# Kernel tuning notes

Measured on AMD Instinct MI355X. Metric: run time of the kernel, lower is better.

## Reference

```python
import jax, jax.numpy as jnp
import numpy as np

D = 128      # embedding_dim
H = 8        # n_heads
L = 2        # n_encode_layers
FF = 512     # feed-forward hidden (4*D, AM default)
CLIP = 10.0  # tanh_clipping
EPS = 1e-5


def setup_inputs() -> dict:
    key = jax.random.key(0)
    ks = jax.random.split(key, 24)
    B, N = 32, 1000
    Nt = N + 2  # 2 depots + customers

    def w(k, shape, fan_in):
        return (jax.random.normal(k, shape, jnp.float32) / np.float32(np.sqrt(fan_in)))

    inp = {}
    inp["depot"] = jax.random.uniform(ks[0], (B, 2, 2), jnp.float32)
    inp["loc"] = jax.random.uniform(ks[1], (B, N, 2), jnp.float32)
    inp["demand"] = jax.random.uniform(ks[2], (B, N), jnp.float32)
    inp["mask"] = jax.random.randint(ks[3], (B, Nt), 0, 2) == 1
    # init embeddings
    inp["W_init_node"] = w(ks[4], (3, D), 3)
    inp["b_init_node"] = jnp.zeros((D,), jnp.float32)
    inp["W_init_depot"] = w(ks[5], (2, D), 2)
    inp["b_init_depot"] = jnp.zeros((D,), jnp.float32)
    # encoder layers (stacked over L)
    inp["enc_Wqkv"] = w(ks[6], (L, D, 3 * D), D)
    inp["enc_Wo"] = w(ks[7], (L, D, D), D)
    inp["enc_W1"] = w(ks[8], (L, D, FF), D)
    inp["enc_b1"] = jnp.zeros((L, FF), jnp.float32)
    inp["enc_W2"] = w(ks[9], (L, FF, D), FF)
    inp["enc_b2"] = jnp.zeros((L, D), jnp.float32)
    inp["bn1_s"] = jnp.ones((L, D), jnp.float32)
    inp["bn1_b"] = jnp.zeros((L, D), jnp.float32)
    inp["bn2_s"] = jnp.ones((L, D), jnp.float32)
    inp["bn2_b"] = jnp.zeros((L, D), jnp.float32)
    # decoder precompute / pointer attention
    inp["W_proj_node"] = w(ks[10], (D, 3 * D), D)   # project_node_embeddings_p2v
    inp["W_fixed_ctx"] = w(ks[11], (D, D), D)       # project_node_query_context
    inp["W_step_ctx"] = w(ks[12], (D, D), D)        # project_step_context_p2v
    inp["W_out"] = w(ks[13], (D, D), D)             # project_out_p2v
    return inp


def _bn(x, s, b):
    # BatchNorm1d over flattened (batch*nodes), training-mode stats, affine
    m = x.mean((0, 1))
    v = x.var((0, 1))
    return s * (x - m) * jax.lax.rsqrt(v + EPS) + b


def _mha(x, Wqkv, Wo):
    B, N, _ = x.shape
    dk = D // H
    q, k, v = jnp.split(x @ Wqkv, 3, axis=-1)

    def heads(t):
        return t.reshape(B, N, H, dk).transpose(0, 2, 1, 3)  # [B,H,N,dk]

    q, k, v = heads(q), heads(k), heads(v)
    attn = jax.nn.softmax(jnp.einsum('bhqd,bhkd->bhqk', q, k) / np.float32(np.sqrt(dk)), axis=-1)
    o = jnp.einsum('bhqk,bhkd->bhqd', attn, v).transpose(0, 2, 1, 3).reshape(B, N, D)
    return o @ Wo


def reference(depot, loc, demand, mask,
              W_init_node, b_init_node, W_init_depot, b_init_depot,
              enc_Wqkv, enc_Wo, enc_W1, enc_b1, enc_W2, enc_b2,
              bn1_s, bn1_b, bn2_s, bn2_b,
              W_proj_node, W_fixed_ctx, W_step_ctx, W_out):
    B = loc.shape[0]
    NEG = jnp.float32(-1e9)
    # --- init embeddings: depots via Linear(2,D), nodes via Linear(3,D) on (x,y,demand)
    depot_emb = depot @ W_init_depot + b_init_depot                      # [B,2,D]
    node_feat = jnp.concatenate([loc, demand[..., None]], -1)            # [B,N,3]
    node_emb = node_feat @ W_init_node + b_init_node                     # [B,N,D]
    h = jnp.concatenate([depot_emb, node_emb], 1)                        # [B,Nt,D]
    # --- graph encoder: L x (MHA + BN skip, FF + BN skip)
    for l in range(L):
        h = _bn(h + _mha(h, enc_Wqkv[l], enc_Wo[l]), bn1_s[l], bn1_b[l])
        ff = jax.nn.relu(h @ enc_W1[l] + enc_b1[l]) @ enc_W2[l] + enc_b2[l]
        h = _bn(h + ff, bn2_s[l], bn2_b[l])
    # --- fixed precompute (AttentionModelFixed)
    graph_embed = h.mean(1)                                              # [B,D]
    fixed_ctx = graph_embed @ W_fixed_ctx                                # [B,D]
    K_g, V_g, K_logit = jnp.split(h @ W_proj_node, 3, axis=-1)           # each [B,Nt,D]
    dk = D // H
    Kh = K_g.reshape(B, -1, H, dk).transpose(0, 2, 1, 3)                 # [B,H,Nt,dk]
    Vh = V_g.reshape(B, -1, H, dk).transpose(0, 2, 1, 3)
    # --- one glimpse+pointer step: context = fixed + projected first-depot step context
    query = fixed_ctx + h[:, 0, :] @ W_step_ctx                          # [B,D]
    qh = query.reshape(B, H, dk)                                         # [B,H,dk]
    compat = jnp.einsum('bhd,bhnd->bhn', qh, Kh) / np.float32(np.sqrt(dk))
    compat = jnp.where(mask[:, None, :], NEG, compat)                    # mask_inner
    attn = jax.nn.softmax(compat, axis=-1)
    glimpse = jnp.einsum('bhn,bhnd->bhd', attn, Vh).reshape(B, D) @ W_out
    logits = jnp.einsum('bd,bnd->bn', glimpse, K_logit) / np.float32(np.sqrt(D))
    logits = CLIP * jnp.tanh(logits)                                     # tanh clipping
    logits = jnp.where(mask, NEG, logits)                                # mask_logits
    log_p = jax.nn.log_softmax(logits, axis=-1)                          # [B,Nt]
    return log_p
```

## Files before the change

### kernel.cpp

```cpp
#include <hip/hip_runtime.h>

#define B_   32
#define NT_  1002
#define D_   128
#define H_   8
#define FF_  512
#define ROWS (B_ * NT_)
#define NEGV (-1e9f)
#define NTP  1024

typedef __bf16 bf16;
typedef __bf16 bf16x8 __attribute__((ext_vector_type(8)));
typedef __bf16 bf16x4 __attribute__((ext_vector_type(4)));
typedef float  f32x4  __attribute__((ext_vector_type(4)));
typedef float  f32x16 __attribute__((ext_vector_type(16)));

#if __has_builtin(__builtin_amdgcn_exp2f)
#define EXP2(x) __builtin_amdgcn_exp2f(x)
#else
#define EXP2(x) exp2f(x)
#endif

#define SZ_QKV (2*384*128)
#define SZ_WO  (2*128*128)
#define SZ_W1  (2*512*128)
#define SZ_W2  (2*128*512)
#define SZ_PROJ (384*128)

__global__ __launch_bounds__(256) void prep_w(
    const float* __restrict__ qkv, const float* __restrict__ wo, const float* __restrict__ w1,
    const float* __restrict__ w2, const float* __restrict__ proj, bf16* __restrict__ out) {
  int i = blockIdx.x * 256 + threadIdx.x;
  int j = i;
  float v;
  if (j < SZ_QKV) {
    int l = j / 49152, r = j % 49152; int n = r >> 7, k = r & 127;
    v = qkv[((size_t)l * 128 + k) * 384 + n];
  } else {
    j -= SZ_QKV;
    if (j < SZ_WO) {
      int l = j >> 14, r = j & 16383; int n = r >> 7, k = r & 127;
      v = wo[((size_t)l * 128 + k) * 128 + n];
    } else {
      j -= SZ_WO;
      if (j < SZ_W1) {
        int l = j >> 16, r = j & 65535; int n = r >> 7, k = r & 127;
        v = w1[((size_t)l * 128 + k) * 512 + n];
      } else {
        j -= SZ_W1;
        if (j < SZ_W2) {
          int l = j >> 16, r = j & 65535; int n = r >> 9, k = r & 511;
          v = w2[((size_t)l * 512 + k) * 128 + n];
        } else {
          j -= SZ_W2;
          int n = j >> 7, k = j & 127;
          v = proj[(size_t)k * 384 + n];
        }
      }
    }
  }
  out[i] = (bf16)v;
}

__global__ __launch_bounds__(256) void init_kernel(
    const float* __restrict__ depot, const float* __restrict__ loc, const float* __restrict__ demand,
    const float* __restrict__ Wn, const float* __restrict__ bn_, const float* __restrict__ Wd,
    const float* __restrict__ bd, bf16* __restrict__ hb) {
  int idx = blockIdx.x * 256 + threadIdx.x;
  if (idx >= ROWS * D_) return;
  int c = idx & 127;
  int row = idx >> 7;
  int b = row / NT_;
  int n = row - b * NT_;
  float v;
  if (n < 2) {
    const float* dp = depot + (b * 2 + n) * 2;
    v = dp[0] * Wd[c] + dp[1] * Wd[D_ + c] + bd[c];
  } else {
    int i = n - 2;
    const float* lp = loc + ((size_t)b * 1000 + i) * 2;
    v = lp[0] * Wn[c] + lp[1] * Wn[D_ + c] + demand[b * 1000 + i] * Wn[2 * D_ + c] + bn_[c];
  }
  hb[idx] = (bf16)v;
}

template<int N_, int K_, bool OUTBF, bool BIAS, bool RELU, bool RES, bool STATS>
__global__ __launch_bounds__(256) void mgemm(
    const bf16* __restrict__ A, const bf16* __restrict__ Wt,
    const float* __restrict__ bias, const bf16* __restrict__ R, void* __restrict__ Cout,
    float* __restrict__ ps, float* __restrict__ pq) {
  __shared__ bf16 As[64][40];
  __shared__ bf16 Bs[64][40];
  __shared__ float sredS[4][32];
  __shared__ float sredQ[4][32];
  int tid = threadIdx.x;
  int w = tid >> 6, l = tid & 63;
  int bm = blockIdx.y * 64, bn = blockIdx.x * 64;
  int wr = (w >> 1) * 32, wc = (w & 1) * 32;
  f32x4 acc[2][2] = {};
  int sr = tid >> 2, ss = (tid & 3) * 8;
  for (int k0 = 0; k0 < K_; k0 += 32) {
    __syncthreads();
    *(bf16x8*)&As[sr][ss] = *(const bf16x8*)&A[(size_t)(bm + sr) * K_ + k0 + ss];
    *(bf16x8*)&Bs[sr][ss] = *(const bf16x8*)&Wt[(size_t)(bn + sr) * K_ + k0 + ss];
    __syncthreads();
    bf16x8 af[2], bfr[2];
#pragma unroll
    for (int mi = 0; mi < 2; ++mi) af[mi] = *(const bf16x8*)&As[wr + mi * 16 + (l & 15)][(l >> 4) * 8];
#pragma unroll
    for (int ni = 0; ni < 2; ++ni) bfr[ni] = *(const bf16x8*)&Bs[wc + ni * 16 + (l & 15)][(l >> 4) * 8];
#pragma unroll
    for (int mi = 0; mi < 2; ++mi)
#pragma unroll
      for (int ni = 0; ni < 2; ++ni)
        acc[mi][ni] = __builtin_amdgcn_mfma_f32_16x16x32_bf16(af[mi], bfr[ni], acc[mi][ni], 0, 0, 0);
  }
  float scol[2] = {0.f, 0.f}, qcol[2] = {0.f, 0.f};
#pragma unroll
  for (int mi = 0; mi < 2; ++mi)
#pragma unroll
    for (int ni = 0; ni < 2; ++ni)
#pragma unroll
      for (int r = 0; r < 4; ++r) {
        int row = bm + wr + mi * 16 + (l >> 4) * 4 + r;
        int col = bn + wc + ni * 16 + (l & 15);
        float v = acc[mi][ni][r];
        if (BIAS) v += bias[col];
        if (RELU) v = fmaxf(v, 0.f);
        if (RES)  v += (float)R[(size_t)row * N_ + col];
        if (STATS) { scol[ni] += v; qcol[ni] += v * v; }
        if (OUTBF) ((bf16*)Cout)[(size_t)row * N_ + col] = (bf16)v;
        else       ((float*)Cout)[(size_t)row * N_ + col] = v;
      }
  if (STATS) {
#pragma unroll
    for (int ni = 0; ni < 2; ++ni) {
      scol[ni] += __shfl_xor(scol[ni], 16); scol[ni] += __shfl_xor(scol[ni], 32);
      qcol[ni] += __shfl_xor(qcol[ni], 16); qcol[ni] += __shfl_xor(qcol[ni], 32);
    }
    __syncthreads();
    if (l < 16) {
#pragma unroll
      for (int ni = 0; ni < 2; ++ni) {
        sredS[w][ni * 16 + l] = scol[ni];
        sredQ[w][ni * 16 + l] = qcol[ni];
      }
    }
    __syncthreads();
    if (tid < 64) {
      int c = tid, hf = c >> 5, cc = c & 31;
      ps[(size_t)(bn + c) * 512 + blockIdx.y] = sredS[hf][cc] + sredS[hf + 2][cc];
      pq[(size_t)(bn + c) * 512 + blockIdx.y] = sredQ[hf][cc] + sredQ[hf + 2][cc];
    }
  }
}

__global__ __launch_bounds__(256) void mgemm_qkv(
    const bf16* __restrict__ A, const bf16* __restrict__ Wt,
    bf16* __restrict__ Qh, bf16* __restrict__ Kh, bf16* __restrict__ Vh) {
  __shared__ bf16 As[64][40];
  __shared__ bf16 Bs[64][40];
  __shared__ bf16 Vt[64][68];
  int tid = threadIdx.x;
  int w = tid >> 6, l = tid & 63;
  int bm = blockIdx.y * 64, bn = blockIdx.x * 64;
  int wr = (w >> 1) * 32, wc = (w & 1) * 32;
  f32x4 acc[2][2] = {};
  int sr = tid >> 2, ss = (tid & 3) * 8;
  for (int k0 = 0; k0 < 128; k0 += 32) {
    __syncthreads();
    *(bf16x8*)&As[sr][ss] = *(const bf16x8*)&A[(size_t)(bm + sr) * 128 + k0 + ss];
    *(bf16x8*)&Bs[sr][ss] = *(const bf16x8*)&Wt[(size_t)(bn + sr) * 128 + k0 + ss];
    __syncthreads();
    bf16x8 af[2], bfr[2];
#pragma unroll
    for (int mi = 0; mi < 2; ++mi) af[mi] = *(const bf16x8*)&As[wr + mi * 16 + (l & 15)][(l >> 4) * 8];
#pragma unroll
    for (int ni = 0; ni < 2; ++ni) bfr[ni] = *(const bf16x8*)&Bs[wc + ni * 16 + (l & 15)][(l >> 4) * 8];
#pragma unroll
    for (int mi = 0; mi < 2; ++mi)
#pragma unroll
      for (int ni = 0; ni < 2; ++ni)
        acc[mi][ni] = __builtin_amdgcn_mfma_f32_16x16x32_bf16(af[mi], bfr[ni], acc[mi][ni], 0, 0, 0);
  }
  if (blockIdx.x < 4) {
#pragma unroll
    for (int ni = 0; ni < 2; ++ni) {
      int col = bn + wc + ni * 16 + (l & 15);
      bf16* dst = (col < 128) ? Qh : Kh;
      int hd = (col >> 4) & 7, c16 = col & 15;
#pragma unroll
      for (int mi = 0; mi < 2; ++mi)
#pragma unroll
        for (int r = 0; r < 4; ++r) {
          int row = bm + wr + mi * 16 + (l >> 4) * 4 + r;
          int b = row / NT_;
          int n = row - b * NT_;
          dst[(((size_t)b * 8 + hd) * NTP + n) * 16 + c16] = (bf16)acc[mi][ni][r];
        }
    }
  } else {
    __syncthreads();
#pragma unroll
    for (int mi = 0; mi < 2; ++mi)
#pragma unroll
      for (int ni = 0; ni < 2; ++ni)
#pragma unroll
        for (int r = 0; r < 4; ++r)
          Vt[wr + mi * 16 + (l >> 4) * 4 + r][wc + ni * 16 + (l & 15)] = (bf16)acc[mi][ni][r];
    __syncthreads();
    int colg = tid >> 4;
    int nl = tid & 15;
#pragma unroll
    for (int ci = 0; ci < 4; ++ci) {
      int lc = colg + ci * 16;
      int gcol = bn + lc;
      int hd = (gcol >> 4) & 7, c16 = gcol & 15;
#pragma unroll
      for (int ri = 0; ri < 4; ++ri) {
        int lrow = nl + ri * 16;
        int row = bm + lrow;
        int b = row / NT_;
        int n = row - b * NT_;
        Vh[(((size_t)b * 8 + hd) * 16 + c16) * NTP + n] = Vt[lrow][lc];
      }
    }
  }
}

__global__ __launch_bounds__(256) void mattn(
    const bf16* __restrict__ Qh, const bf16* __restrict__ Kh,
    const bf16* __restrict__ Vh, bf16* __restrict__ ab) {
  __shared__ bf16 KsF[1024];
  __shared__ bf16 VtF[1024];
  __shared__ bf16 PsF[4][2048];
  int tid = threadIdx.x;
  int w = tid >> 6, l = tid & 63;
  int bh = blockIdx.x;
  int b = bh >> 3, hd = bh & 7;
  const bf16* Qp = Qh + (size_t)bh * NTP * 16;
  const bf16* Kp = Kh + (size_t)bh * NTP * 16;
  const bf16* Vp = Vh + (size_t)bh * 16 * NTP;
  int qbase = blockIdx.y * 128 + w * 32;
  int qrow = qbase + (l & 31); if (qrow >= NT_) qrow = NT_ - 1;
  bf16x8 qf = *(const bf16x8*)&Qp[qrow * 16 + (l >> 5) * 8];

  const float SC = 0.25f * 1.44269504088896f;
  const float MC = 8.0f * SC;
  f32x4 oacc[2] = {};
  f32x4 lacc[2] = {};
  bf16x8 ones;
#pragma unroll
  for (int i = 0; i < 8; ++i) ones[i] = (bf16)1.0f;
  const f32x16 zz = {0,0,0,0,0,0,0,0,0,0,0,0,0,0,0,0};

  for (int t = 0; t < 16; ++t) {
    int kb = t * 64;
    __syncthreads();
    if (tid < 128) {
      int key = (tid >> 6) * 32 + (tid & 31);
      int h2 = (tid >> 5) & 1;
      int krow = kb + key; if (krow >= NT_) krow = NT_ - 1;
      *(bf16x8*)&KsF[tid * 8] = *(const bf16x8*)&Kp[krow * 16 + h2 * 8];
    } else {
      int u = tid - 128;
      int seg = u >> 4, dim = u & 15;
      *(bf16x8*)&VtF[u * 8] = *(const bf16x8*)&Vp[dim * NTP + kb + seg * 8];
    }
    __syncthreads();

    f32x16 sv[2];
#pragma unroll
    for (int c = 0; c < 2; ++c) {
      bf16x8 kf = *(const bf16x8*)&KsF[(c * 64 + l) * 8];
      sv[c] = __builtin_amdgcn_mfma_f32_32x32x16_bf16(kf, qf, zz, 0, 0, 0);
    }
    if (kb + 64 > NT_) {
#pragma unroll
      for (int c = 0; c < 2; ++c)
#pragma unroll
        for (int r = 0; r < 16; ++r) {
          int key = kb + c * 32 + (r & 3) + 8 * (r >> 2) + 4 * (l >> 5);
          if (key >= NT_) sv[c][r] = -1e30f;
        }
    }
#pragma unroll
    for (int c = 0; c < 2; ++c)
#pragma unroll
      for (int r = 0; r < 16; ++r)
        sv[c][r] = EXP2(__builtin_fmaf(sv[c][r], SC, -MC));
    {
      int q = l & 31;
      int qh4 = q >> 4, ql = q & 15, half = (l >> 5) * 4;
#pragma unroll
      for (int c = 0; c < 2; ++c)
#pragma unroll
        for (int g2 = 0; g2 < 4; ++g2) {
          bf16x4 pk;
#pragma unroll
          for (int i = 0; i < 4; ++i) pk[i] = (bf16)sv[c][g2 * 4 + i];
          int unit = (c * 2 + qh4) * 64 + g2 * 16 + ql;
          *(bf16x4*)&PsF[w][unit * 8 + half] = pk;
        }
    }
#pragma unroll
    for (int kh = 0; kh < 2; ++kh) {
      bf16x8 vf = *(const bf16x8*)&VtF[(kh * 64 + l) * 8];
#pragma unroll
      for (int g = 0; g < 2; ++g) {
        bf16x8 pf = *(const bf16x8*)&PsF[w][((kh * 2 + g) * 64 + l) * 8];
        oacc[g] = __builtin_amdgcn_mfma_f32_16x16x32_bf16(pf, vf, oacc[g], 0, 0, 0);
        lacc[g] = __builtin_amdgcn_mfma_f32_16x16x32_bf16(pf, ones, lacc[g], 0, 0, 0);
      }
    }
  }
#pragma unroll
  for (int g = 0; g < 2; ++g)
#pragma unroll
    for (int r = 0; r < 4; ++r) {
      int qq = qbase + g * 16 + (l >> 4) * 4 + r;
      if (qq < NT_)
        ab[((size_t)b * NT_ + qq) * 128 + hd * 16 + (l & 15)] = (bf16)(oacc[g][r] / lacc[g][r]);
    }
}

__global__ __launch_bounds__(512) void stats_final(
    const float* __restrict__ ps, const float* __restrict__ pq,
    const float* __restrict__ sc, const float* __restrict__ bi, float* __restrict__ mi) {
  int tid = threadIdx.x;
  int c = tid >> 2, q4 = tid & 3;
  float s = 0.f, q = 0.f;
  for (int p = q4; p < 501; p += 4) { s += ps[c * 512 + p]; q += pq[c * 512 + p]; }
  s += __shfl_xor(s, 1); s += __shfl_xor(s, 2);
  q += __shfl_xor(q, 1); q += __shfl_xor(q, 2);
  if (q4 == 0) {
    float mean = s * (1.f / (float)ROWS);
    float var = q * (1.f / (float)ROWS) - mean * mean;
    float s2 = sc[c] * rsqrtf(var + 1e-5f);
    mi[c] = s2;
    mi[128 + c] = bi[c] - mean * s2;
  }
}

__global__ __launch_bounds__(256) void bn_apply(const bf16* __restrict__ X, const float* __restrict__ mi,
                                                bf16* __restrict__ Y) {
  __shared__ float sS[128], sB[128];
  if (threadIdx.x < 128) { sS[threadIdx.x] = mi[threadIdx.x]; sB[threadIdx.x] = mi[128 + threadIdx.x]; }
  __syncthreads();
  int chunk = blockIdx.x * 256 + threadIdx.x;
  if (chunk < ROWS * 16) {
    int c0 = (chunk & 15) * 8;
    bf16x8 x = *(const bf16x8*)&X[(size_t)chunk * 8];
    bf16x8 y;
#pragma unroll
    for (int i = 0; i < 8; ++i) y[i] = (bf16)__builtin_fmaf((float)x[i], sS[c0 + i], sB[c0 + i]);
    *(bf16x8*)&Y[(size_t)chunk * 8] = y;
  }
}

__global__ void ge_partial(const bf16* __restrict__ hb, float* __restrict__ part) {
  int b = blockIdx.x, ch = blockIdx.y, d = threadIdx.x;
  int n0 = ch * 126, n1 = n0 + 126; if (n1 > NT_) n1 = NT_;
  float s = 0.f;
  for (int n = n0; n < n1; ++n) s += (float)hb[((size_t)b * NT_ + n) * D_ + d];
  part[(b * 8 + ch) * D_ + d] = s;
}

__global__ void query_kernel(const float* __restrict__ part, const bf16* __restrict__ hb,
                             const float* __restrict__ Wf, const float* __restrict__ Ws,
                             float* __restrict__ qry) {
  __shared__ float sge[128], sh0[128];
  int b = blockIdx.x, d = threadIdx.x;
  float s = 0.f;
#pragma unroll
  for (int ch = 0; ch < 8; ++ch) s += part[(b * 8 + ch) * D_ + d];
  sge[d] = s * (1.f / (float)NT_);
  sh0[d] = (float)hb[(size_t)b * NT_ * D_ + d];
  __syncthreads();
  float q = 0.f;
  for (int k = 0; k < 128; ++k) q += sge[k] * Wf[k * D_ + d] + sh0[k] * Ws[k * D_ + d];
  qry[b * D_ + d] = q;
}

__global__ __launch_bounds__(256) void glimpse_kernel(
    const bf16* __restrict__ proj, const float* __restrict__ qry,
    const int* __restrict__ mask, float* __restrict__ glimpse) {
  int bid = blockIdx.x; int b = bid >> 3, hd = bid & 7;
  int tid = threadIdx.x;
  __shared__ float sq[16];
  __shared__ float sex[NT_];
  __shared__ float rmax[4];
  __shared__ float wacc[4][17];
  if (tid < 16) sq[tid] = qry[b * 128 + hd * 16 + tid];
  __syncthreads();
  const bf16* P = proj + (size_t)b * NT_ * 384;
  const int* Mk = mask + b * NT_;
  float lmax = -1e30f;
#pragma unroll
  for (int it = 0; it < 4; ++it) {
    int n = tid + it * 256;
    if (n < NT_) {
      float c = NEGV;
      if (!Mk[n]) {
        const bf16* kp = &P[(size_t)n * 384 + hd * 16];
        bf16x8 k0 = *(const bf16x8*)kp, k1 = *(const bf16x8*)(kp + 8);
        float d = 0.f;
#pragma unroll
        for (int i = 0; i < 8; ++i) d += sq[i] * (float)k0[i] + sq[8 + i] * (float)k1[i];
        c = d * 0.25f;
      }
      sex[n] = c;
      lmax = fmaxf(lmax, c);
    }
  }
#pragma unroll
  for (int o = 32; o > 0; o >>= 1) lmax = fmaxf(lmax, __shfl_xor(lmax, o));
  if ((tid & 63) == 0) rmax[tid >> 6] = lmax;
  __syncthreads();
  float mx = fmaxf(fmaxf(rmax[0], rmax[1]), fmaxf(rmax[2], rmax[3]));
  float acc[16];
#pragma unroll
  for (int i = 0; i < 16; ++i) acc[i] = 0.f;
  float lsum = 0.f;
#pragma unroll
  for (int it = 0; it < 4; ++it) {
    int n = tid + it * 256;
    if (n < NT_) {
      float e = __expf(sex[n] - mx);
      lsum += e;
      const bf16* vp = &P[(size_t)n * 384 + 128 + hd * 16];
      bf16x8 v0 = *(const bf16x8*)vp, v1 = *(const bf16x8*)(vp + 8);
#pragma unroll
      for (int i = 0; i < 8; ++i) { acc[i] += e * (float)v0[i]; acc[8 + i] += e * (float)v1[i]; }
    }
  }
#pragma unroll
  for (int o = 32; o > 0; o >>= 1) {
    lsum += __shfl_xor(lsum, o);
#pragma unroll
    for (int i = 0; i < 16; ++i) acc[i] += __shfl_xor(acc[i], o);
  }
  if ((tid & 63) == 0) {
    wacc[tid >> 6][16] = lsum;
#pragma unroll
    for (int i = 0; i < 16; ++i) wacc[tid >> 6][i] = acc[i];
  }
  __syncthreads();
  if (tid < 16) {
    float a = wacc[0][tid] + wacc[1][tid] + wacc[2][tid] + wacc[3][tid];
    float L = wacc[0][16] + wacc[1][16] + wacc[2][16] + wacc[3][16];
    glimpse[b * 128 + hd * 16 + tid] = a / L;
  }
}

__global__ void g2_kernel(const float* __restrict__ glimpse, const float* __restrict__ Wout,
                          float* __restrict__ g2) {
  __shared__ float sg[128];
  int b = blockIdx.x, d = threadIdx.x;
  sg[d] = glimpse[b * 128 + d];
  __syncthreads();
  float s = 0.f;
  for (int k = 0; k < 128; ++k) s += sg[k] * Wout[k * 128 + d];
  g2[b * 128 + d] = s;
}

__global__ __launch_bounds__(256) void logits_kernel(
    const bf16* __restrict__ proj, const float* __restrict__ g2,
    const int* __restrict__ mask, float* __restrict__ logits) {
  int b = blockIdx.y;
  int n = blockIdx.x * 256 + threadIdx.x;
  __shared__ float sg[128];
  if (threadIdx.x < 128) sg[threadIdx.x] = g2[b * 128 + threadIdx.x];
  __syncthreads();
  if (n >= NT_) return;
  const bf16* kp = &proj[((size_t)b * NT_ + n) * 384 + 256];
  float d = 0.f;
#pragma unroll
  for (int j = 0; j < 16; ++j) {
    bf16x8 v = *(const bf16x8*)&kp[j * 8];
#pragma unroll
    for (int i = 0; i < 8; ++i) d += sg[j * 8 + i] * (float)v[i];
  }
  d = 10.f * tanhf(d * 0.088388347648318447f);
  logits[b * NT_ + n] = mask[b * NT_ + n] ? NEGV : d;
}

__global__ __launch_bounds__(256) void lsm_kernel(const float* __restrict__ logits, float* __restrict__ out) {
  int b = blockIdx.x, tid = threadIdx.x;
  __shared__ float red[256];
  float mx = -1e30f;
  for (int n = tid; n < NT_; n += 256) mx = fmaxf(mx, logits[b * NT_ + n]);
  red[tid] = mx; __syncthreads();
  for (int s = 128; s > 0; s >>= 1) { if (tid < s) red[tid] = fmaxf(red[tid], red[tid + s]); __syncthreads(); }
  mx = red[0]; __syncthreads();
  float sm = 0.f;
  for (int n = tid; n < NT_; n += 256) sm += __expf(logits[b * NT_ + n] - mx);
  red[tid] = sm; __syncthreads();
  for (int s = 128; s > 0; s >>= 1) { if (tid < s) red[tid] += red[tid + s]; __syncthreads(); }
  float lse = mx + logf(red[0]);
  for (int n = tid; n < NT_; n += 256) out[(size_t)b * NT_ + n] = logits[b * NT_ + n] - lse;
}

extern "C" void kernel_launch(void* const* d_in, const int* in_sizes, int n_in,
                              void* d_out, int out_size, void* d_ws, size_t ws_size,
                              hipStream_t stream) {
  const float* depot        = (const float*)d_in[0];
  const float* loc          = (const float*)d_in[1];
  const float* demand       = (const float*)d_in[2];
  const int*   mask         = (const int*)d_in[3];
  const float* W_init_node  = (const float*)d_in[4];
  const float* b_init_node  = (const float*)d_in[5];
  const float* W_init_depot = (const float*)d_in[6];
  const float* b_init_depot = (const float*)d_in[7];
  const float* enc_Wqkv     = (const float*)d_in[8];
  const float* enc_Wo       = (const float*)d_in[9];
  const float* enc_W1       = (const float*)d_in[10];
  const float* enc_b1       = (const float*)d_in[11];
  const float* enc_W2       = (const float*)d_in[12];
  const float* enc_b2       = (const float*)d_in[13];
  const float* bn1_s        = (const float*)d_in[14];
  const float* bn1_b        = (const float*)d_in[15];
  const float* bn2_s        = (const float*)d_in[16];
  const float* bn2_b        = (const float*)d_in[17];
  const float* W_proj       = (const float*)d_in[18];
  const float* W_fixed      = (const float*)d_in[19];
  const float* W_step       = (const float*)d_in[20];
  const float* W_out        = (const float*)d_in[21];
  float* out = (float*)d_out;

  char* base = (char*)d_ws;
  bf16*  hb    = (bf16*)(base);
  bf16*  ab    = (bf16*)(base + 8208384);
  bf16*  Qh    = (bf16*)(base + 16416768);
  bf16*  Kh    = (bf16*)(base + 24805376);
  bf16*  Vh    = (bf16*)(base + 33193984);
  bf16*  xb    = Qh;
  bf16*  projb = Qh;
  bf16*  ff1b  = (bf16*)(base + 41582592);
  bf16*  wb    = (bf16*)(base + 74416128);
  float* ps    = (float*)(base + 75300864);
  float* pq    = (float*)(base + 75563008);
  float* mi    = (float*)(base + 75825152);
  float* qry   = (float*)(base + 75826176);
  float* glim  = (float*)(base + 75842560);
  float* g2    = (float*)(base + 75858944);
  float* gep   = ps;
  float* logit = pq;

  bf16* wt_qkv  = wb;
  bf16* wt_wo   = wb + SZ_QKV;
  bf16* wt_w1   = wb + SZ_QKV + SZ_WO;
  bf16* wt_w2   = wb + SZ_QKV + SZ_WO + SZ_W1;
  bf16* wt_proj = wb + SZ_QKV + SZ_WO + SZ_W1 + SZ_W2;

  prep_w<<<1728, 256, 0, stream>>>(enc_Wqkv, enc_Wo, enc_W1, enc_W2, W_proj, wb);
  init_kernel<<<(ROWS * D_ + 255) / 256, 256, 0, stream>>>(
      depot, loc, demand, W_init_node, b_init_node, W_init_depot, b_init_depot, hb);

  for (int l = 0; l < 2; ++l) {
    mgemm_qkv<<<dim3(6, 501), 256, 0, stream>>>(
        hb, wt_qkv + (size_t)l * 384 * 128, Qh, Kh, Vh);
    mattn<<<dim3(256, 8), 256, 0, stream>>>(Qh, Kh, Vh, ab);
    mgemm<128, 128, true, false, false, true, true><<<dim3(2, 501), 256, 0, stream>>>(
        ab, wt_wo + (size_t)l * 128 * 128, nullptr, hb, xb, ps, pq);
    stats_final<<<1, 512, 0, stream>>>(ps, pq, bn1_s + l * D_, bn1_b + l * D_, mi);
    bn_apply<<<2004, 256, 0, stream>>>(xb, mi, hb);
    mgemm<512, 128, true, true, true, false, false><<<dim3(8, 501), 256, 0, stream>>>(
        hb, wt_w1 + (size_t)l * 512 * 128, enc_b1 + (size_t)l * FF_, nullptr, ff1b, nullptr, nullptr);
    mgemm<128, 512, true, true, false, true, true><<<dim3(2, 501), 256, 0, stream>>>(
        ff1b, wt_w2 + (size_t)l * 128 * 512, enc_b2 + (size_t)l * D_, hb, xb, ps, pq);
    stats_final<<<1, 512, 0, stream>>>(ps, pq, bn2_s + l * D_, bn2_b + l * D_, mi);
    bn_apply<<<2004, 256, 0, stream>>>(xb, mi, hb);
  }

  mgemm<384, 128, true, false, false, false, false><<<dim3(6, 501), 256, 0, stream>>>(
      hb, wt_proj, nullptr, nullptr, projb, nullptr, nullptr);
  ge_partial<<<dim3(32, 8), 128, 0, stream>>>(hb, gep);
  query_kernel<<<32, 128, 0, stream>>>(gep, hb, W_fixed, W_step, qry);
  glimpse_kernel<<<256, 256, 0, stream>>>(projb, qry, mask, glim);
  g2_kernel<<<32, 128, 0, stream>>>(glim, W_out, g2);
  logits_kernel<<<dim3(4, 32), 256, 0, stream>>>(projb, g2, mask, logit);
  lsm_kernel<<<32, 256, 0, stream>>>(logit, out);
}
```

Baseline: 423.6 us.

## Widen GEMM tiles to 64x128 with fragment-ordered shared layout

Grows the N tile of the generic GEMM and the QKV GEMM from 64 to 128 columns, so each wave computes 2x4 MFMA tiles instead of 2x2 and each A tile is reused across twice as many columns. Shared memory is rearranged into an MFMA-fragment-ordered unit layout with no padding, meant to avoid bank conflicts on the bf16x8 fragment reads. The V transpose now packs four bf16 values per shared store. Grids halve, which lowers the number of blocks, and the larger accumulators raise register pressure and may reduce occupancy.

```diff
diff --git a/kernel.cpp b/kernel.cpp
--- a/kernel.cpp
+++ b/kernel.cpp
@@ -20,6 +20,10 @@
 #else
 #define EXP2(x) exp2f(x)
 #endif
+
+__device__ __forceinline__ int UNIT(int row, int seg) {
+  return (row >> 4) * 64 + seg * 16 + (row & 15);
+}
 
 #define SZ_QKV (2*384*128)
 #define SZ_WO  (2*128*128)
@@ -84,42 +88,47 @@
   hb[idx] = (bf16)v;
 }
 
-template<int N_, int K_, bool OUTBF, bool BIAS, bool RELU, bool RES, bool STATS>
+template<int N_, int K_, bool BIAS, bool RELU, bool RES, bool STATS>
 __global__ __launch_bounds__(256) void mgemm(
     const bf16* __restrict__ A, const bf16* __restrict__ Wt,
-    const float* __restrict__ bias, const bf16* __restrict__ R, void* __restrict__ Cout,
+    const float* __restrict__ bias, const bf16* __restrict__ R, bf16* __restrict__ Cout,
     float* __restrict__ ps, float* __restrict__ pq) {
-  __shared__ bf16 As[64][40];
-  __shared__ bf16 Bs[64][40];
-  __shared__ float sredS[4][32];
-  __shared__ float sredQ[4][32];
+  __shared__ bf16 AsF[2048];
+  __shared__ bf16 BsF[4096];
+  __shared__ float sredS[4][64];
+  __shared__ float sredQ[4][64];
   int tid = threadIdx.x;
   int w = tid >> 6, l = tid & 63;
-  int bm = blockIdx.y * 64, bn = blockIdx.x * 64;
-  int wr = (w >> 1) * 32, wc = (w & 1) * 32;
-  f32x4 acc[2][2] = {};
-  int sr = tid >> 2, ss = (tid & 3) * 8;
+  int bm = blockIdx.y * 64, bn = blockIdx.x * 128;
+  int wr = (w >> 1) * 32, wc = (w & 1) * 64;
+  f32x4 acc[2][4] = {};
+  int srow = tid >> 2, sseg = tid & 3;
+  int uA = UNIT(srow, sseg);
+  int uB0 = UNIT(srow, sseg), uB1 = UNIT(srow + 64, sseg);
   for (int k0 = 0; k0 < K_; k0 += 32) {
     __syncthreads();
-    *(bf16x8*)&As[sr][ss] = *(const bf16x8*)&A[(size_t)(bm + sr) * K_ + k0 + ss];
-    *(bf16x8*)&Bs[sr][ss] = *(const bf16x8*)&Wt[(size_t)(bn + sr) * K_ + k0 + ss];
-    __syncthreads();
-    bf16x8 af[2], bfr[2];
-#pragma unroll
-    for (int mi = 0; mi < 2; ++mi) af[mi] = *(const bf16x8*)&As[wr + mi * 16 + (l & 15)][(l >> 4) * 8];
-#pragma unroll
-    for (int ni = 0; ni < 2; ++ni) bfr[ni] = *(const bf16x8*)&Bs[wc + ni * 16 + (l & 15)][(l >> 4) * 8];
+    *(bf16x8*)&AsF[uA * 8] = *(const bf16x8*)&A[(size_t)(bm + srow) * K_ + k0 + sseg * 8];
+    *(bf16x8*)&BsF[uB0 * 8] = *(const bf16x8*)&Wt[(size_t)(bn + srow) * K_ + k0 + sseg * 8];
+    *(bf16x8*)&BsF[uB1 * 8] = *(const bf16x8*)&Wt[(size_t)(bn + srow + 64) * K_ + k0 + sseg * 8];
+    __syncthreads();
+    bf16x8 af[2], bfr[4];
 #pragma unroll
     for (int mi = 0; mi < 2; ++mi)
-#pragma unroll
-      for (int ni = 0; ni < 2; ++ni)
+      af[mi] = *(const bf16x8*)&AsF[(((wr >> 4) + mi) * 64 + (l >> 4) * 16 + (l & 15)) * 8];
+#pragma unroll
+    for (int ni = 0; ni < 4; ++ni)
+      bfr[ni] = *(const bf16x8*)&BsF[(((wc >> 4) + ni) * 64 + (l >> 4) * 16 + (l & 15)) * 8];
+#pragma unroll
+    for (int mi = 0; mi < 2; ++mi)
+#pragma unroll
+      for (int ni = 0; ni < 4; ++ni)
         acc[mi][ni] = __builtin_amdgcn_mfma_f32_16x16x32_bf16(af[mi], bfr[ni], acc[mi][ni], 0, 0, 0);
   }
-  float scol[2] = {0.f, 0.f}, qcol[2] = {0.f, 0.f};
+  float scol[4] = {}, qcol[4] = {};
 #pragma unroll
   for (int mi = 0; mi < 2; ++mi)
 #pragma unroll
-    for (int ni = 0; ni < 2; ++ni)
+    for (int ni = 0; ni < 4; ++ni)
 #pragma unroll
       for (int r = 0; r < 4; ++r) {
         int row = bm + wr + mi * 16 + (l >> 4) * 4 + r;
@@ -129,28 +138,27 @@
         if (RELU) v = fmaxf(v, 0.f);
         if (RES)  v += (float)R[(size_t)row * N_ + col];
         if (STATS) { scol[ni] += v; qcol[ni] += v * v; }
-        if (OUTBF) ((bf16*)Cout)[(size_t)row * N_ + col] = (bf16)v;
-        else       ((float*)Cout)[(size_t)row * N_ + col] = v;
+        Cout[(size_t)row * N_ + col] = (bf16)v;
       }
   if (STATS) {
 #pragma unroll
-    for (int ni = 0; ni < 2; ++ni) {
+    for (int ni = 0; ni < 4; ++ni) {
       scol[ni] += __shfl_xor(scol[ni], 16); scol[ni] += __shfl_xor(scol[ni], 32);
       qcol[ni] += __shfl_xor(qcol[ni], 16); qcol[ni] += __shfl_xor(qcol[ni], 32);
     }
     __syncthreads();
     if (l < 16) {
 #pragma unroll
-      for (int ni = 0; ni < 2; ++ni) {
+      for (int ni = 0; ni < 4; ++ni) {
         sredS[w][ni * 16 + l] = scol[ni];
         sredQ[w][ni * 16 + l] = qcol[ni];
       }
     }
     __syncthreads();
-    if (tid < 64) {
-      int c = tid, hf = c >> 5, cc = c & 31;
-      ps[(size_t)(bn + c) * 512 + blockIdx.y] = sredS[hf][cc] + sredS[hf + 2][cc];
-      pq[(size_t)(bn + c) * 512 + blockIdx.y] = sredQ[hf][cc] + sredQ[hf + 2][cc];
+    if (tid < 128) {
+      int c = tid, cw = c >> 6, cc = c & 63;
+      ps[(size_t)(bn + c) * 512 + blockIdx.y] = sredS[cw][cc] + sredS[cw + 2][cc];
+      pq[(size_t)(bn + c) * 512 + blockIdx.y] = sredQ[cw][cc] + sredQ[cw + 2][cc];
     }
   }
 }
@@ -158,37 +166,43 @@
 __global__ __launch_bounds__(256) void mgemm_qkv(
     const bf16* __restrict__ A, const bf16* __restrict__ Wt,
     bf16* __restrict__ Qh, bf16* __restrict__ Kh, bf16* __restrict__ Vh) {
-  __shared__ bf16 As[64][40];
-  __shared__ bf16 Bs[64][40];
-  __shared__ bf16 Vt[64][68];
+  __shared__ bf16 smem[128 * 68];
+  bf16* AsF = smem;
+  bf16* BsF = smem + 2048;
+  bf16* Vt2 = smem;
   int tid = threadIdx.x;
   int w = tid >> 6, l = tid & 63;
-  int bm = blockIdx.y * 64, bn = blockIdx.x * 64;
-  int wr = (w >> 1) * 32, wc = (w & 1) * 32;
-  f32x4 acc[2][2] = {};
-  int sr = tid >> 2, ss = (tid & 3) * 8;
+  int bm = blockIdx.y * 64, bn = blockIdx.x * 128;
+  int wr = (w >> 1) * 32, wc = (w & 1) * 64;
+  f32x4 acc[2][4] = {};
+  int srow = tid >> 2, sseg = tid & 3;
+  int uA = UNIT(srow, sseg);
+  int uB0 = UNIT(srow, sseg), uB1 = UNIT(srow + 64, sseg);
   for (int k0 = 0; k0 < 128; k0 += 32) {
     __syncthreads();
-    *(bf16x8*)&As[sr][ss] = *(const bf16x8*)&A[(size_t)(bm + sr) * 128 + k0 + ss];
-    *(bf16x8*)&Bs[sr][ss] = *(const bf16x8*)&Wt[(size_t)(bn + sr) * 128 + k0 + ss];
-    __syncthreads();
-    bf16x8 af[2], bfr[2];
-#pragma unroll
-    for (int mi = 0; mi < 2; ++mi) af[mi] = *(const bf16x8*)&As[wr + mi * 16 + (l & 15)][(l >> 4) * 8];
-#pragma unroll
-    for (int ni = 0; ni < 2; ++ni) bfr[ni] = *(const bf16x8*)&Bs[wc + ni * 16 + (l & 15)][(l >> 4) * 8];
+    *(bf16x8*)&AsF[uA * 8] = *(const bf16x8*)&A[(size_t)(bm + srow) * 128 + k0 + sseg * 8];
+    *(bf16x8*)&BsF[uB0 * 8] = *(const bf16x8*)&Wt[(size_t)(bn + srow) * 128 + k0 + sseg * 8];
+    *(bf16x8*)&BsF[uB1 * 8] = *(const bf16x8*)&Wt[(size_t)(bn + srow + 64) * 128 + k0 + sseg * 8];
+    __syncthreads();
+    bf16x8 af[2], bfr[4];
 #pragma unroll
     for (int mi = 0; mi < 2; ++mi)
-#pragma unroll
-      for (int ni = 0; ni < 2; ++ni)
+      af[mi] = *(const bf16x8*)&AsF[(((wr >> 4) + mi) * 64 + (l >> 4) * 16 + (l & 15)) * 8];
+#pragma unroll
+    for (int ni = 0; ni < 4; ++ni)
+      bfr[ni] = *(const bf16x8*)&BsF[(((wc >> 4) + ni) * 64 + (l >> 4) * 16 + (l & 15)) * 8];
+#pragma unroll
+    for (int mi = 0; mi < 2; ++mi)
+#pragma unroll
+      for (int ni = 0; ni < 4; ++ni)
         acc[mi][ni] = __builtin_amdgcn_mfma_f32_16x16x32_bf16(af[mi], bfr[ni], acc[mi][ni], 0, 0, 0);
   }
-  if (blockIdx.x < 4) {
-#pragma unroll
-    for (int ni = 0; ni < 2; ++ni) {
-      int col = bn + wc + ni * 16 + (l & 15);
-      bf16* dst = (col < 128) ? Qh : Kh;
-      int hd = (col >> 4) & 7, c16 = col & 15;
+  if (blockIdx.x < 2) {
+    bf16* dst = (blockIdx.x == 0) ? Qh : Kh;
+#pragma unroll
+    for (int ni = 0; ni < 4; ++ni) {
+      int cl = wc + ni * 16 + (l & 15);
+      int hd = cl >> 4, c16 = cl & 15;
 #pragma unroll
       for (int mi = 0; mi < 2; ++mi)
 #pragma unroll
@@ -204,25 +218,27 @@
 #pragma unroll
     for (int mi = 0; mi < 2; ++mi)
 #pragma unroll
-      for (int ni = 0; ni < 2; ++ni)
-#pragma unroll
-        for (int r = 0; r < 4; ++r)
-          Vt[wr + mi * 16 + (l >> 4) * 4 + r][wc + ni * 16 + (l & 15)] = (bf16)acc[mi][ni][r];
-    __syncthreads();
-    int colg = tid >> 4;
-    int nl = tid & 15;
-#pragma unroll
-    for (int ci = 0; ci < 4; ++ci) {
+      for (int ni = 0; ni < 4; ++ni) {
+        int cl = wc + ni * 16 + (l & 15);
+        int r0 = wr + mi * 16 + (l >> 4) * 4;
+        bf16x4 pk;
+#pragma unroll
+        for (int r = 0; r < 4; ++r) pk[r] = (bf16)acc[mi][ni][r];
+        *(bf16x4*)&Vt2[cl * 68 + r0] = pk;
+      }
+    __syncthreads();
+    int colg = tid >> 4, nl = tid & 15;
+#pragma unroll
+    for (int ci = 0; ci < 8; ++ci) {
       int lc = colg + ci * 16;
-      int gcol = bn + lc;
-      int hd = (gcol >> 4) & 7, c16 = gcol & 15;
+      int hd = lc >> 4, c16 = lc & 15;
 #pragma unroll
       for (int ri = 0; ri < 4; ++ri) {
         int lrow = nl + ri * 16;
         int row = bm + lrow;
         int b = row / NT_;
         int n = row - b * NT_;
-        Vh[(((size_t)b * 8 + hd) * 16 + c16) * NTP + n] = Vt[lrow][lc];
+        Vh[(((size_t)b * 8 + hd) * 16 + c16) * NTP + n] = Vt2[lc * 68 + lrow];
       }
     }
   }
@@ -558,22 +574,22 @@
       depot, loc, demand, W_init_node, b_init_node, W_init_depot, b_init_depot, hb);
 
   for (int l = 0; l < 2; ++l) {
-    mgemm_qkv<<<dim3(6, 501), 256, 0, stream>>>(
+    mgemm_qkv<<<dim3(3, 501), 256, 0, stream>>>(
         hb, wt_qkv + (size_t)l * 384 * 128, Qh, Kh, Vh);
     mattn<<<dim3(256, 8), 256, 0, stream>>>(Qh, Kh, Vh, ab);
-    mgemm<128, 128, true, false, false, true, true><<<dim3(2, 501), 256, 0, stream>>>(
+    mgemm<128, 128, false, false, true, true><<<dim3(1, 501), 256, 0, stream>>>(
         ab, wt_wo + (size_t)l * 128 * 128, nullptr, hb, xb, ps, pq);
     stats_final<<<1, 512, 0, stream>>>(ps, pq, bn1_s + l * D_, bn1_b + l * D_, mi);
     bn_apply<<<2004, 256, 0, stream>>>(xb, mi, hb);
-    mgemm<512, 128, true, true, true, false, false><<<dim3(8, 501), 256, 0, stream>>>(
+    mgemm<512, 128, true, true, false, false><<<dim3(4, 501), 256, 0, stream>>>(
         hb, wt_w1 + (size_t)l * 512 * 128, enc_b1 + (size_t)l * FF_, nullptr, ff1b, nullptr, nullptr);
-    mgemm<128, 512, true, true, false, true, true><<<dim3(2, 501), 256, 0, stream>>>(
+    mgemm<128, 512, true, false, true, true><<<dim3(1, 501), 256, 0, stream>>>(
         ff1b, wt_w2 + (size_t)l * 128 * 512, enc_b2 + (size_t)l * D_, hb, xb, ps, pq);
     stats_final<<<1, 512, 0, stream>>>(ps, pq, bn2_s + l * D_, bn2_b + l * D_, mi);
     bn_apply<<<2004, 256, 0, stream>>>(xb, mi, hb);
   }
 
-  mgemm<384, 128, true, false, false, false, false><<<dim3(6, 501), 256, 0, stream>>>(
+  mgemm<384, 128, false, false, false, false><<<dim3(3, 501), 256, 0, stream>>>(
       hb, wt_proj, nullptr, nullptr, projb, nullptr, nullptr);
   ge_partial<<<dim3(32, 8), 128, 0, stream>>>(hb, gep);
   query_kernel<<<32, 128, 0, stream>>>(gep, hb, W_fixed, W_step, qry);
```

Result: no change. 416.8 us (-1.6%).
